# Optimization experiments

Measured on AMD Instinct MI355X. Metric: run time of the kernel, lower is better.

The kernel has to match this reference:

```python
import jax, jax.numpy as jnp
import numpy as np

IN_CH = 128
OUT_CH = 128
MODES = 16
T = 32
N = 32768
SCALE = 1.0 / (IN_CH * OUT_CH)  # TIME_CONV mode


def setup_inputs() -> dict:
    key = jax.random.key(0)
    k_x, k_w = jax.random.split(key)
    x = jax.random.normal(k_x, (T, N, IN_CH), dtype=jnp.float32)
    # nn.Parameter(scale * torch.rand(in, out, modes, 2)) — real/imag stacked in last dim
    weights = SCALE * jax.random.uniform(k_w, (IN_CH, OUT_CH, MODES, 2), dtype=jnp.float32)
    return {"x": x, "weights": weights}


def reference(x, weights):
    # x: [T, N, C_in]; weights: [C_in, C_out, modes, 2]
    w_c = weights[..., 0] + 1j * weights[..., 1]           # [i, o, m] complex
    x_ft = jnp.fft.rfft(x, axis=0)                          # [T//2+1, N, C_in] complex
    out_ft = jnp.einsum('mni,iom->mno', x_ft[:MODES], w_c)  # [modes, N, C_out] complex
    out = jnp.fft.irfft(out_ft, n=T, axis=0)                # [T, N, C_out] real
    return out
```

## Files before the change

kernel.cpp:

```cpp
#include <hip/hip_runtime.h>
#include <math.h>

typedef short bf16x8 __attribute__((ext_vector_type(8)));
typedef float f32x4  __attribute__((ext_vector_type(4)));

#define TT 32
#define MM 16
#define CC 128
#define NPT 32768
#define NC 4194304
#define BN 16

#define XF_OFF   0
#define OF_OFF   131072
#define OF_STRIDE 80
#define DT_OFF   151552
#define TABC_OFF 153600
#define TABS_OFF 155648
#define LDS_BYTES 157696

static __device__ __forceinline__ unsigned short f2bf(float f) {
    union { float f; unsigned u; } v; v.f = f;
    unsigned r = v.u + 0x7FFFu + ((v.u >> 16) & 1u);
    return (unsigned short)(r >> 16);
}

__global__ void repack_w(const float* __restrict__ w, bf16x8* __restrict__ wb) {
    int r = blockIdx.x * blockDim.x + threadIdx.x;
    int lane = r & 63;
    int r2 = r >> 6;
    int ot = r2 & 7;
    int r3 = r2 >> 3;
    int ck = r3 & 7;
    int r4 = r3 >> 3;
    int ri = r4 & 1;
    int m  = r4 >> 1;
    int o = ot * 16 + (lane & 15);
    int kbase = ck * 32 + (lane >> 4) * 8;
    bf16x8 v;
    #pragma unroll
    for (int j = 0; j < 8; ++j) {
        int k = kbase + j;
        int i = k >> 1, ko = k & 1;
        const float* wp = w + ((size_t)(i * 128 + o) * 16 + m) * 2;
        float val;
        if (ri == 0) val = ko ? -wp[1] : wp[0];
        else         val = ko ?  wp[0] : wp[1];
        v[j] = (short)f2bf(val);
    }
    wb[r] = v;
}

__global__ __launch_bounds__(1024, 2)
void spectral_mfma(const float* __restrict__ x, const bf16x8* __restrict__ wb,
                   float* __restrict__ out) {
    extern __shared__ char lds[];
    float* tabc = (float*)(lds + TABC_OFF);
    float* tabs = (float*)(lds + TABS_OFF);
    const int tid = threadIdx.x;
    const int n0  = blockIdx.x * BN;

    if (tid < 512) {
        int m = tid & 15, t = tid >> 4;
        float ang = 0.19634954084936207f * (float)((m * t) & 31);
        float s, c; sincosf(ang, &s, &c);
        tabc[t * 16 + m] = c;
        tabs[t * 16 + m] = s;
    }
    {
        int t = tid >> 5, k2 = tid & 31, m = k2 >> 1, ri = k2 & 1;
        float alpha = (m == 0) ? 0.03125f : 0.0625f;
        float ang = 0.19634954084936207f * (float)((m * t) & 31);
        float s, c; sincosf(ang, &s, &c);
        float val = (ri == 0) ? alpha * c : -alpha * s;
        if (m == 0 && ri == 1) val = 0.f;
        *(unsigned short*)(lds + DT_OFF + t * 64 + k2 * 2) = f2bf(val);
    }
    __syncthreads();

    {
        const int i2 = (tid & 63) * 2;
        const int nn = tid >> 6;
        const float* xp = x + (size_t)(n0 + nn) * CC + i2;
        float2 x0  = *(const float2*)(xp);
        float2 x16 = *(const float2*)(xp + (size_t)16 * NC);
        float xrA[16], xiA[16], xrB[16], xiB[16];
        #pragma unroll
        for (int m = 0; m < 16; ++m) {
            float sgn = (m & 1) ? -1.f : 1.f;
            xrA[m] = x0.x + sgn * x16.x;
            xrB[m] = x0.y + sgn * x16.y;
            xiA[m] = 0.f; xiB[m] = 0.f;
        }
        #pragma unroll 3
        for (int t = 1; t <= 15; ++t) {
            float2 a = *(const float2*)(xp + (size_t)t * NC);
            float2 b = *(const float2*)(xp + (size_t)(32 - t) * NC);
            float ex = a.x + b.x, ey = a.y + b.y;
            float ox = a.x - b.x, oy = a.y - b.y;
            float4 c0 = *(const float4*)&tabc[t * 16 + 0];
            float4 c1 = *(const float4*)&tabc[t * 16 + 4];
            float4 c2 = *(const float4*)&tabc[t * 16 + 8];
            float4 c3 = *(const float4*)&tabc[t * 16 + 12];
            float4 s0 = *(const float4*)&tabs[t * 16 + 0];
            float4 s1 = *(const float4*)&tabs[t * 16 + 4];
            float4 s2 = *(const float4*)&tabs[t * 16 + 8];
            float4 s3 = *(const float4*)&tabs[t * 16 + 12];
            float cm[16] = {c0.x,c0.y,c0.z,c0.w, c1.x,c1.y,c1.z,c1.w,
                            c2.x,c2.y,c2.z,c2.w, c3.x,c3.y,c3.z,c3.w};
            float sm[16] = {s0.x,s0.y,s0.z,s0.w, s1.x,s1.y,s1.z,s1.w,
                            s2.x,s2.y,s2.z,s2.w, s3.x,s3.y,s3.z,s3.w};
            #pragma unroll
            for (int m = 0; m < 16; ++m) {
                xrA[m] += ex * cm[m]; xrB[m] += ey * cm[m];
                xiA[m] -= ox * sm[m]; xiB[m] -= oy * sm[m];
            }
        }
        char* xfb = lds + XF_OFF;
        #pragma unroll
        for (int m = 0; m < 16; ++m) {
            unsigned byte = (unsigned)(m * 8192 + nn * 512 + i2 * 4);
            byte ^= (unsigned)((nn & 7) << 4);
            uint2 v;
            v.x = (unsigned)f2bf(xrA[m]) | ((unsigned)f2bf(xiA[m]) << 16);
            v.y = (unsigned)f2bf(xrB[m]) | ((unsigned)f2bf(xiB[m]) << 16);
            *(uint2*)(xfb + byte) = v;
        }
    }
    __syncthreads();

    const int lane = tid & 63;
    const int wid  = tid >> 6;
    const int col  = lane & 15;
    const int kq   = lane >> 4;

    bf16x8 afrag[8];
    {
        char* xfb = lds + XF_OFF;
        const unsigned row = (unsigned)(wid * 8192 + col * 512 + kq * 16);
        const unsigned swz = (unsigned)((col & 7) << 4);
        #pragma unroll
        for (int ck = 0; ck < 8; ++ck) {
            unsigned addr = (row + (unsigned)(ck * 64)) ^ swz;
            afrag[ck] = *(const bf16x8*)(xfb + addr);
        }
    }
    bf16x8 dtf0, dtf1;
    {
        char* dtb = lds + DT_OFF;
        dtf0 = *(const bf16x8*)(dtb + col * 64 + kq * 16);
        dtf1 = *(const bf16x8*)(dtb + (col + 16) * 64 + kq * 16);
    }

    char* ofb = lds + OF_OFF;
    float* outp = out + (size_t)(n0 + wid) * CC + col;

    for (int og = 0; og < 8; ++og) {
        f32x4 accR = {0.f, 0.f, 0.f, 0.f};
        f32x4 accI = {0.f, 0.f, 0.f, 0.f};
        #pragma unroll
        for (int ck = 0; ck < 8; ++ck) {
            bf16x8 bR = wb[(((wid * 2 + 0) * 8 + ck) * 8 + og) * 64 + lane];
            bf16x8 bI = wb[(((wid * 2 + 1) * 8 + ck) * 8 + og) * 64 + lane];
            accR = __builtin_amdgcn_mfma_f32_16x16x32_bf16(afrag[ck], bR, accR, 0, 0, 0);
            accI = __builtin_amdgcn_mfma_f32_16x16x32_bf16(afrag[ck], bI, accI, 0, 0, 0);
        }
        #pragma unroll
        for (int j = 0; j < 4; ++j) {
            int no = (kq * 4 + j) * 16 + col;
            unsigned byte = (unsigned)(no * OF_STRIDE + wid * 4);
            unsigned v = (unsigned)f2bf(accR[j]) | ((unsigned)f2bf(accI[j]) << 16);
            *(unsigned*)(ofb + byte) = v;
        }
        __syncthreads();
        {
            int no0 = wid * 16 + col;
            bf16x8 pf = *(const bf16x8*)(ofb + no0 * OF_STRIDE + kq * 16);
            f32x4 z = {0.f, 0.f, 0.f, 0.f};
            f32x4 c0 = __builtin_amdgcn_mfma_f32_16x16x32_bf16(dtf0, pf, z, 0, 0, 0);
            f32x4 c1 = __builtin_amdgcn_mfma_f32_16x16x32_bf16(dtf1, pf, z, 0, 0, 0);
            float* op = outp + og * 16;
            #pragma unroll
            for (int j = 0; j < 4; ++j) {
                int t0 = kq * 4 + j;
                op[(size_t)t0 * NC]        = c0[j];
                op[(size_t)(t0 + 16) * NC] = c1[j];
            }
        }
        __syncthreads();
    }
}

#define FBN 8
#define FXST 36
__global__ __launch_bounds__(512, 2)
void spectral_fused(const float* __restrict__ x,
                    const float* __restrict__ w,
                    float* __restrict__ out) {
    extern __shared__ float flds[];
    float* xf    = flds;
    float* ftabc = flds + FBN * CC * FXST;
    float* ftabs = ftabc + 512;

    const int tid = threadIdx.x;
    const int n0  = blockIdx.x * FBN;

    {
        const int m = tid >> 5;
        const int t = tid & 31;
        const int k = (m * t) & 31;
        const float ang = 0.19634954084936207f * (float)k;
        float s, c; sincosf(ang, &s, &c);
        ftabc[tid] = c; ftabs[tid] = s;
    }
    __syncthreads();
    {
        const int i   = tid & 127;
        const int nnA = tid >> 7;
        const int nnB = nnA + 4;
        float xra[MM], xia[MM], xrb[MM], xib[MM];
        #pragma unroll
        for (int m = 0; m < MM; ++m) { xra[m]=0.f; xia[m]=0.f; xrb[m]=0.f; xib[m]=0.f; }
        const float* xA = x + (size_t)(n0 + nnA) * CC + i;
        const float* xB = x + (size_t)(n0 + nnB) * CC + i;
        for (int t = 0; t < TT; ++t) {
            const float va = xA[(size_t)t * NC];
            const float vb = xB[(size_t)t * NC];
            #pragma unroll
            for (int m = 0; m < MM; ++m) {
                const float c = ftabc[(m << 5) + t];
                const float s = ftabs[(m << 5) + t];
                xra[m] += va * c;  xia[m] -= va * s;
                xrb[m] += vb * c;  xib[m] -= vb * s;
            }
        }
        float* dA = xf + (size_t)(nnA * CC + i) * FXST;
        float* dB = xf + (size_t)(nnB * CC + i) * FXST;
        #pragma unroll
        for (int j = 0; j < 8; ++j) {
            *(float4*)(dA + 4 * j) = make_float4(xra[2*j], xia[2*j], xra[2*j+1], xia[2*j+1]);
            *(float4*)(dB + 4 * j) = make_float4(xrb[2*j], xib[2*j], xrb[2*j+1], xib[2*j+1]);
        }
    }
    __syncthreads();
    const int o   = tid & 127;
    const int nnA = tid >> 7;
    const int nnB = nnA + 4;
    float ar[MM], ai_[MM], br[MM], bi_[MM];
    #pragma unroll
    for (int m = 0; m < MM; ++m) { ar[m]=0.f; ai_[m]=0.f; br[m]=0.f; bi_[m]=0.f; }
    const float* qa0 = xf + (size_t)(nnA * CC) * FXST;
    const float* qb0 = xf + (size_t)(nnB * CC) * FXST;
    float4 wv[8];
    {
        const float4* wp = (const float4*)(w + (size_t)o * 32);
        #pragma unroll
        for (int j = 0; j < 8; ++j) wv[j] = wp[j];
    }
    for (int i = 0; i < CC; ++i) {
        float4 xa4[8], xb4[8];
        const float4* qa = (const float4*)(qa0 + i * FXST);
        const float4* qb = (const float4*)(qb0 + i * FXST);
        #pragma unroll
        for (int j = 0; j < 8; ++j) { xa4[j] = qa[j]; xb4[j] = qb[j]; }
        float4 wn[8];
        if (i + 1 < CC) {
            const float4* wp = (const float4*)(w + (size_t)((i + 1) * CC + o) * 32);
            #pragma unroll
            for (int j = 0; j < 8; ++j) wn[j] = wp[j];
        }
        #pragma unroll
        for (int j = 0; j < 8; ++j) {
            const int m0 = 2 * j, m1 = 2 * j + 1;
            ar[m0]  += xa4[j].x * wv[j].x - xa4[j].y * wv[j].y;
            ai_[m0] += xa4[j].x * wv[j].y + xa4[j].y * wv[j].x;
            br[m0]  += xb4[j].x * wv[j].x - xb4[j].y * wv[j].y;
            bi_[m0] += xb4[j].x * wv[j].y + xb4[j].y * wv[j].x;
            ar[m1]  += xa4[j].z * wv[j].z - xa4[j].w * wv[j].w;
            ai_[m1] += xa4[j].z * wv[j].w + xa4[j].w * wv[j].z;
            br[m1]  += xb4[j].z * wv[j].z - xb4[j].w * wv[j].w;
            bi_[m1] += xb4[j].z * wv[j].w + xb4[j].w * wv[j].z;
        }
        #pragma unroll
        for (int j = 0; j < 8; ++j) wv[j] = wn[j];
    }
    {
        const float inv = 1.0f / 32.0f;
        const size_t obA = (size_t)(n0 + nnA) * CC + o;
        const size_t obB = (size_t)(n0 + nnB) * CC + o;
        for (int t = 0; t < TT; ++t) {
            float accA = 0.f, accB = 0.f;
            #pragma unroll
            for (int m = 1; m < MM; ++m) {
                const float c = ftabc[(m << 5) + t];
                const float s = ftabs[(m << 5) + t];
                accA += ar[m] * c - ai_[m] * s;
                accB += br[m] * c - bi_[m] * s;
            }
            out[(size_t)t * NC + obA] = (ar[0] + 2.f * accA) * inv;
            out[(size_t)t * NC + obB] = (br[0] + 2.f * accB) * inv;
        }
    }
}

extern "C" void kernel_launch(void* const* d_in, const int* in_sizes, int n_in,
                              void* d_out, int out_size, void* d_ws, size_t ws_size,
                              hipStream_t stream) {
    (void)in_sizes; (void)n_in; (void)out_size;
    const float* x = (const float*)d_in[0];
    const float* w = (const float*)d_in[1];
    float* out     = (float*)d_out;

    if (d_ws != nullptr && ws_size >= (size_t)2 * 1024 * 1024) {
        bf16x8* wbuf = (bf16x8*)d_ws;
        hipLaunchKernelGGL(repack_w, dim3(512), dim3(256), 0, stream, w, wbuf);
        hipLaunchKernelGGL(spectral_mfma, dim3(NPT / BN), dim3(1024), LDS_BYTES, stream,
                           x, wbuf, out);
    } else {
        const size_t lds_bytes = (size_t)(FBN * CC * FXST + 1024) * sizeof(float);
        hipLaunchKernelGGL(spectral_fused, dim3(NPT / FBN), dim3(512), lds_bytes, stream,
                           x, w, out);
    }
}
```

Baseline: 464.7 us.

## Halve block tile to 8 points, shrink LDS and registers for higher occupancy

Reduces the per-block point count from 16 to 8, roughly halving LDS use and per-thread DFT register arrays so more blocks can be resident per CU (launch bounds raised to 8). The weight layout is reordered so each wave streams a contiguous og-major slab, A fragments are loaded from LDS per ck instead of being held in registers, and the inverse-DFT matrix is computed in registers with each half of the waves producing 16 time steps. In exchange the grid doubles, weights are reloaded twice as often per point, and half the lanes go idle during the spectral write-out.

```diff
diff --git a/kernel.cpp b/kernel.cpp
--- a/kernel.cpp
+++ b/kernel.cpp
@@ -9,15 +9,14 @@
 #define CC 128
 #define NPT 32768
 #define NC 4194304
-#define BN 16
+#define BN 8
 
 #define XF_OFF   0
-#define OF_OFF   131072
+#define OF_OFF   65536
 #define OF_STRIDE 80
-#define DT_OFF   151552
-#define TABC_OFF 153600
-#define TABS_OFF 155648
-#define LDS_BYTES 157696
+#define TABC_OFF 75776
+#define TABS_OFF 77824
+#define LDS_BYTES 79872
 
 static __device__ __forceinline__ unsigned short f2bf(float f) {
     union { float f; unsigned u; } v; v.f = f;
@@ -29,13 +28,13 @@
     int r = blockIdx.x * blockDim.x + threadIdx.x;
     int lane = r & 63;
     int r2 = r >> 6;
-    int ot = r2 & 7;
+    int ck = r2 & 7;
     int r3 = r2 >> 3;
-    int ck = r3 & 7;
-    int r4 = r3 >> 3;
-    int ri = r4 & 1;
-    int m  = r4 >> 1;
-    int o = ot * 16 + (lane & 15);
+    int ri = r3 & 1;
+    int r4 = r3 >> 1;
+    int og = r4 & 7;
+    int m  = r4 >> 3;
+    int o = og * 16 + (lane & 15);
     int kbase = ck * 32 + (lane >> 4) * 8;
     bf16x8 v;
     #pragma unroll
@@ -51,7 +50,7 @@
     wb[r] = v;
 }
 
-__global__ __launch_bounds__(1024, 2)
+__global__ __launch_bounds__(1024, 8)
 void spectral_mfma(const float* __restrict__ x, const bf16x8* __restrict__ wb,
                    float* __restrict__ out) {
     extern __shared__ char lds[];
@@ -67,124 +66,110 @@
         tabc[t * 16 + m] = c;
         tabs[t * 16 + m] = s;
     }
-    {
-        int t = tid >> 5, k2 = tid & 31, m = k2 >> 1, ri = k2 & 1;
-        float alpha = (m == 0) ? 0.03125f : 0.0625f;
-        float ang = 0.19634954084936207f * (float)((m * t) & 31);
-        float s, c; sincosf(ang, &s, &c);
-        float val = (ri == 0) ? alpha * c : -alpha * s;
-        if (m == 0 && ri == 1) val = 0.f;
-        *(unsigned short*)(lds + DT_OFF + t * 64 + k2 * 2) = f2bf(val);
-    }
     __syncthreads();
 
     {
-        const int i2 = (tid & 63) * 2;
-        const int nn = tid >> 6;
-        const float* xp = x + (size_t)(n0 + nn) * CC + i2;
-        float2 x0  = *(const float2*)(xp);
-        float2 x16 = *(const float2*)(xp + (size_t)16 * NC);
-        float xrA[16], xiA[16], xrB[16], xiB[16];
+        const int i  = tid & 127;
+        const int nn = tid >> 7;
+        const float* xp = x + (size_t)(n0 + nn) * CC + i;
+        float x0  = xp[0];
+        float x16 = xp[(size_t)16 * NC];
+        float xr[16], xi[16];
         #pragma unroll
         for (int m = 0; m < 16; ++m) {
-            float sgn = (m & 1) ? -1.f : 1.f;
-            xrA[m] = x0.x + sgn * x16.x;
-            xrB[m] = x0.y + sgn * x16.y;
-            xiA[m] = 0.f; xiB[m] = 0.f;
-        }
-        #pragma unroll 3
+            xr[m] = x0 + ((m & 1) ? -x16 : x16);
+            xi[m] = 0.f;
+        }
+        #pragma unroll
         for (int t = 1; t <= 15; ++t) {
-            float2 a = *(const float2*)(xp + (size_t)t * NC);
-            float2 b = *(const float2*)(xp + (size_t)(32 - t) * NC);
-            float ex = a.x + b.x, ey = a.y + b.y;
-            float ox = a.x - b.x, oy = a.y - b.y;
-            float4 c0 = *(const float4*)&tabc[t * 16 + 0];
-            float4 c1 = *(const float4*)&tabc[t * 16 + 4];
-            float4 c2 = *(const float4*)&tabc[t * 16 + 8];
-            float4 c3 = *(const float4*)&tabc[t * 16 + 12];
-            float4 s0 = *(const float4*)&tabs[t * 16 + 0];
-            float4 s1 = *(const float4*)&tabs[t * 16 + 4];
-            float4 s2 = *(const float4*)&tabs[t * 16 + 8];
-            float4 s3 = *(const float4*)&tabs[t * 16 + 12];
-            float cm[16] = {c0.x,c0.y,c0.z,c0.w, c1.x,c1.y,c1.z,c1.w,
-                            c2.x,c2.y,c2.z,c2.w, c3.x,c3.y,c3.z,c3.w};
-            float sm[16] = {s0.x,s0.y,s0.z,s0.w, s1.x,s1.y,s1.z,s1.w,
-                            s2.x,s2.y,s2.z,s2.w, s3.x,s3.y,s3.z,s3.w};
-            #pragma unroll
-            for (int m = 0; m < 16; ++m) {
-                xrA[m] += ex * cm[m]; xrB[m] += ey * cm[m];
-                xiA[m] -= ox * sm[m]; xiB[m] -= oy * sm[m];
+            float a = xp[(size_t)t * NC];
+            float b = xp[(size_t)(32 - t) * NC];
+            float e = a + b, od = a - b;
+            #pragma unroll
+            for (int mh = 0; mh < 16; mh += 8) {
+                float4 c0 = *(const float4*)&tabc[t * 16 + mh];
+                float4 c1 = *(const float4*)&tabc[t * 16 + mh + 4];
+                float4 s0 = *(const float4*)&tabs[t * 16 + mh];
+                float4 s1 = *(const float4*)&tabs[t * 16 + mh + 4];
+                xr[mh+0] += e * c0.x;  xi[mh+0] -= od * s0.x;
+                xr[mh+1] += e * c0.y;  xi[mh+1] -= od * s0.y;
+                xr[mh+2] += e * c0.z;  xi[mh+2] -= od * s0.z;
+                xr[mh+3] += e * c0.w;  xi[mh+3] -= od * s0.w;
+                xr[mh+4] += e * c1.x;  xi[mh+4] -= od * s1.x;
+                xr[mh+5] += e * c1.y;  xi[mh+5] -= od * s1.y;
+                xr[mh+6] += e * c1.z;  xi[mh+6] -= od * s1.z;
+                xr[mh+7] += e * c1.w;  xi[mh+7] -= od * s1.w;
             }
         }
         char* xfb = lds + XF_OFF;
         #pragma unroll
         for (int m = 0; m < 16; ++m) {
-            unsigned byte = (unsigned)(m * 8192 + nn * 512 + i2 * 4);
-            byte ^= (unsigned)((nn & 7) << 4);
-            uint2 v;
-            v.x = (unsigned)f2bf(xrA[m]) | ((unsigned)f2bf(xiA[m]) << 16);
-            v.y = (unsigned)f2bf(xrB[m]) | ((unsigned)f2bf(xiB[m]) << 16);
-            *(uint2*)(xfb + byte) = v;
+            unsigned byte = ((unsigned)(m * 4096 + nn * 512 + i * 4))
+                            ^ ((unsigned)(nn & 7) << 4);
+            unsigned v = (unsigned)f2bf(xr[m]) | ((unsigned)f2bf(xi[m]) << 16);
+            *(unsigned*)(xfb + byte) = v;
         }
     }
     __syncthreads();
 
-    const int lane = tid & 63;
-    const int wid  = tid >> 6;
-    const int col  = lane & 15;
-    const int kq   = lane >> 4;
-
-    bf16x8 afrag[8];
-    {
-        char* xfb = lds + XF_OFF;
-        const unsigned row = (unsigned)(wid * 8192 + col * 512 + kq * 16);
-        const unsigned swz = (unsigned)((col & 7) << 4);
-        #pragma unroll
-        for (int ck = 0; ck < 8; ++ck) {
-            unsigned addr = (row + (unsigned)(ck * 64)) ^ swz;
-            afrag[ck] = *(const bf16x8*)(xfb + addr);
-        }
-    }
-    bf16x8 dtf0, dtf1;
-    {
-        char* dtb = lds + DT_OFF;
-        dtf0 = *(const bf16x8*)(dtb + col * 64 + kq * 16);
-        dtf1 = *(const bf16x8*)(dtb + (col + 16) * 64 + kq * 16);
-    }
-
+    const int lane  = tid & 63;
+    const int wid   = tid >> 6;
+    const int col   = lane & 15;
+    const int kq    = lane >> 4;
+    const int thalf = wid >> 3;
+
+    bf16x8 dtf;
+    {
+        const int t = thalf * 16 + col;
+        #pragma unroll
+        for (int jm = 0; jm < 4; ++jm) {
+            int m = kq * 4 + jm;
+            float alpha = (m == 0) ? 0.03125f : 0.0625f;
+            float ang = 0.19634954084936207f * (float)((m * t) & 31);
+            float s, c; sincosf(ang, &s, &c);
+            dtf[jm * 2 + 0] = (short)f2bf(alpha * c);
+            dtf[jm * 2 + 1] = (m == 0) ? (short)0 : (short)f2bf(-alpha * s);
+        }
+    }
+
+    char* xfb = lds + XF_OFF;
     char* ofb = lds + OF_OFF;
-    float* outp = out + (size_t)(n0 + wid) * CC + col;
+    const unsigned arow = (unsigned)(wid * 4096 + (col & 7) * 512 + kq * 16);
+    const unsigned aswz = (unsigned)((col & 7) << 4);
+    const bf16x8* wbase = wb + (size_t)wid * (8 * 2 * 8 * 64);
+    float* outp = out + (size_t)(n0 + (wid & 7)) * CC + col;
 
     for (int og = 0; og < 8; ++og) {
+        const bf16x8* wog = wbase + (size_t)og * (2 * 8 * 64);
         f32x4 accR = {0.f, 0.f, 0.f, 0.f};
         f32x4 accI = {0.f, 0.f, 0.f, 0.f};
         #pragma unroll
         for (int ck = 0; ck < 8; ++ck) {
-            bf16x8 bR = wb[(((wid * 2 + 0) * 8 + ck) * 8 + og) * 64 + lane];
-            bf16x8 bI = wb[(((wid * 2 + 1) * 8 + ck) * 8 + og) * 64 + lane];
-            accR = __builtin_amdgcn_mfma_f32_16x16x32_bf16(afrag[ck], bR, accR, 0, 0, 0);
-            accI = __builtin_amdgcn_mfma_f32_16x16x32_bf16(afrag[ck], bI, accI, 0, 0, 0);
-        }
-        #pragma unroll
-        for (int j = 0; j < 4; ++j) {
-            int no = (kq * 4 + j) * 16 + col;
-            unsigned byte = (unsigned)(no * OF_STRIDE + wid * 4);
-            unsigned v = (unsigned)f2bf(accR[j]) | ((unsigned)f2bf(accI[j]) << 16);
-            *(unsigned*)(ofb + byte) = v;
+            bf16x8 af = *(const bf16x8*)(xfb + ((arow + (unsigned)(ck * 64)) ^ aswz));
+            bf16x8 bR = wog[(0 * 8 + ck) * 64 + lane];
+            bf16x8 bI = wog[(1 * 8 + ck) * 64 + lane];
+            accR = __builtin_amdgcn_mfma_f32_16x16x32_bf16(af, bR, accR, 0, 0, 0);
+            accI = __builtin_amdgcn_mfma_f32_16x16x32_bf16(af, bI, accI, 0, 0, 0);
+        }
+        if (kq < 2) {
+            #pragma unroll
+            for (int j = 0; j < 4; ++j) {
+                int no = (kq * 4 + j) * 16 + col;
+                unsigned v = (unsigned)f2bf(accR[j]) | ((unsigned)f2bf(accI[j]) << 16);
+                *(unsigned*)(ofb + no * OF_STRIDE + wid * 4) = v;
+            }
         }
         __syncthreads();
         {
-            int no0 = wid * 16 + col;
+            int no0 = (wid & 7) * 16 + col;
             bf16x8 pf = *(const bf16x8*)(ofb + no0 * OF_STRIDE + kq * 16);
             f32x4 z = {0.f, 0.f, 0.f, 0.f};
-            f32x4 c0 = __builtin_amdgcn_mfma_f32_16x16x32_bf16(dtf0, pf, z, 0, 0, 0);
-            f32x4 c1 = __builtin_amdgcn_mfma_f32_16x16x32_bf16(dtf1, pf, z, 0, 0, 0);
+            f32x4 cc = __builtin_amdgcn_mfma_f32_16x16x32_bf16(dtf, pf, z, 0, 0, 0);
             float* op = outp + og * 16;
             #pragma unroll
             for (int j = 0; j < 4; ++j) {
-                int t0 = kq * 4 + j;
-                op[(size_t)t0 * NC]        = c0[j];
-                op[(size_t)(t0 + 16) * NC] = c1[j];
+                int t0 = thalf * 16 + kq * 4 + j;
+                op[(size_t)t0 * NC] = cc[j];
             }
         }
         __syncthreads();
```

After: 551.1 us. +18.6%, slower.

## Halve block to 8 points, cut LDS, recompute DFT fragments in registers

Applied to the files above, without the earlier changes.

Shrinks each block to 8 spatial points and 512 threads so LDS use drops to about 76 KB, allowing more blocks per CU. Each wave now handles two modes per output group and loads A fragments from LDS on demand instead of holding all of them in registers. The weight repack order changes to match. The inverse-DFT fragments are computed directly in registers rather than through an LDS table, and output stores for pairs of channel groups are batched together. The costs are more LDS traffic for A fragments, half the waves idle during the spectral writeback, and a tighter synchronisation structure.

```diff
diff --git a/kernel.cpp b/kernel.cpp
--- a/kernel.cpp
+++ b/kernel.cpp
@@ -2,6 +2,7 @@
 #include <math.h>
 
 typedef short bf16x8 __attribute__((ext_vector_type(8)));
+typedef short bf16x4 __attribute__((ext_vector_type(4)));
 typedef float f32x4  __attribute__((ext_vector_type(4)));
 
 #define TT 32
@@ -9,33 +10,34 @@
 #define CC 128
 #define NPT 32768
 #define NC 4194304
-#define BN 16
+#define BN 8
 
 #define XF_OFF   0
-#define OF_OFF   131072
-#define OF_STRIDE 80
-#define DT_OFF   151552
-#define TABC_OFF 153600
-#define TABS_OFF 155648
-#define LDS_BYTES 157696
+#define OF_OFF   65536
+#define TABC_OFF 73728
+#define TABS_OFF 75776
+#define LDS_BYTES 77824
 
 static __device__ __forceinline__ unsigned short f2bf(float f) {
     union { float f; unsigned u; } v; v.f = f;
     unsigned r = v.u + 0x7FFFu + ((v.u >> 16) & 1u);
     return (unsigned short)(r >> 16);
 }
+static __device__ __forceinline__ unsigned pack2(float lo, float hi) {
+    return (unsigned)f2bf(lo) | ((unsigned)f2bf(hi) << 16);
+}
 
 __global__ void repack_w(const float* __restrict__ w, bf16x8* __restrict__ wb) {
     int r = blockIdx.x * blockDim.x + threadIdx.x;
     int lane = r & 63;
     int r2 = r >> 6;
-    int ot = r2 & 7;
+    int ck = r2 & 7;
     int r3 = r2 >> 3;
-    int ck = r3 & 7;
-    int r4 = r3 >> 3;
-    int ri = r4 & 1;
-    int m  = r4 >> 1;
-    int o = ot * 16 + (lane & 15);
+    int ri = r3 & 1;
+    int r4 = r3 >> 1;
+    int og = r4 & 7;
+    int m  = r4 >> 3;
+    int o = og * 16 + (lane & 15);
     int kbase = ck * 32 + (lane >> 4) * 8;
     bf16x8 v;
     #pragma unroll
@@ -51,7 +53,7 @@
     wb[r] = v;
 }
 
-__global__ __launch_bounds__(1024, 2)
+__global__ __launch_bounds__(512, 2)
 void spectral_mfma(const float* __restrict__ x, const bf16x8* __restrict__ wb,
                    float* __restrict__ out) {
     extern __shared__ char lds[];
@@ -60,27 +62,37 @@
     const int tid = threadIdx.x;
     const int n0  = blockIdx.x * BN;
 
-    if (tid < 512) {
+    const int lane = tid & 63;
+    const int wid  = tid >> 6;
+    const int col  = lane & 15;
+    const int kq   = lane >> 4;
+
+    {
         int m = tid & 15, t = tid >> 4;
-        float ang = 0.19634954084936207f * (float)((m * t) & 31);
-        float s, c; sincosf(ang, &s, &c);
+        float s, c;
+        sincosf(0.19634954084936207f * (float)((m * t) & 31), &s, &c);
         tabc[t * 16 + m] = c;
         tabs[t * 16 + m] = s;
     }
-    {
-        int t = tid >> 5, k2 = tid & 31, m = k2 >> 1, ri = k2 & 1;
+
+    bf16x8 dtf0, dtf1;
+    #pragma unroll
+    for (int jm = 0; jm < 4; ++jm) {
+        int m = kq * 4 + jm;
         float alpha = (m == 0) ? 0.03125f : 0.0625f;
-        float ang = 0.19634954084936207f * (float)((m * t) & 31);
-        float s, c; sincosf(ang, &s, &c);
-        float val = (ri == 0) ? alpha * c : -alpha * s;
-        if (m == 0 && ri == 1) val = 0.f;
-        *(unsigned short*)(lds + DT_OFF + t * 64 + k2 * 2) = f2bf(val);
+        float s, c;
+        sincosf(0.19634954084936207f * (float)((m * col) & 31), &s, &c);
+        dtf0[jm * 2 + 0] = (short)f2bf(alpha * c);
+        dtf0[jm * 2 + 1] = (m == 0) ? (short)0 : (short)f2bf(-alpha * s);
+        sincosf(0.19634954084936207f * (float)((m * (col + 16)) & 31), &s, &c);
+        dtf1[jm * 2 + 0] = (short)f2bf(alpha * c);
+        dtf1[jm * 2 + 1] = (m == 0) ? (short)0 : (short)f2bf(-alpha * s);
     }
     __syncthreads();
 
     {
+        const int nn = tid >> 6;
         const int i2 = (tid & 63) * 2;
-        const int nn = tid >> 6;
         const float* xp = x + (size_t)(n0 + nn) * CC + i2;
         float2 x0  = *(const float2*)(xp);
         float2 x16 = *(const float2*)(xp + (size_t)16 * NC);
@@ -112,79 +124,80 @@
                             s2.x,s2.y,s2.z,s2.w, s3.x,s3.y,s3.z,s3.w};
             #pragma unroll
             for (int m = 0; m < 16; ++m) {
-                xrA[m] += ex * cm[m]; xrB[m] += ey * cm[m];
-                xiA[m] -= ox * sm[m]; xiB[m] -= oy * sm[m];
+                xrA[m] += ex * cm[m];  xiA[m] -= ox * sm[m];
+                xrB[m] += ey * cm[m];  xiB[m] -= oy * sm[m];
             }
         }
         char* xfb = lds + XF_OFF;
         #pragma unroll
         for (int m = 0; m < 16; ++m) {
-            unsigned byte = (unsigned)(m * 8192 + nn * 512 + i2 * 4);
-            byte ^= (unsigned)((nn & 7) << 4);
-            uint2 v;
-            v.x = (unsigned)f2bf(xrA[m]) | ((unsigned)f2bf(xiA[m]) << 16);
-            v.y = (unsigned)f2bf(xrB[m]) | ((unsigned)f2bf(xiB[m]) << 16);
-            *(uint2*)(xfb + byte) = v;
+            unsigned byte = ((unsigned)(m * 4096 + nn * 512 + i2 * 4))
+                            ^ ((unsigned)(nn & 7) << 4);
+            uint2 v2;
+            v2.x = pack2(xrA[m], xiA[m]);
+            v2.y = pack2(xrB[m], xiB[m]);
+            *(uint2*)(xfb + byte) = v2;
         }
     }
     __syncthreads();
 
-    const int lane = tid & 63;
-    const int wid  = tid >> 6;
-    const int col  = lane & 15;
-    const int kq   = lane >> 4;
-
-    bf16x8 afrag[8];
-    {
-        char* xfb = lds + XF_OFF;
-        const unsigned row = (unsigned)(wid * 8192 + col * 512 + kq * 16);
-        const unsigned swz = (unsigned)((col & 7) << 4);
-        #pragma unroll
-        for (int ck = 0; ck < 8; ++ck) {
-            unsigned addr = (row + (unsigned)(ck * 64)) ^ swz;
-            afrag[ck] = *(const bf16x8*)(xfb + addr);
-        }
-    }
-    bf16x8 dtf0, dtf1;
-    {
-        char* dtb = lds + DT_OFF;
-        dtf0 = *(const bf16x8*)(dtb + col * 64 + kq * 16);
-        dtf1 = *(const bf16x8*)(dtb + (col + 16) * 64 + kq * 16);
-    }
-
+    char* xfb = lds + XF_OFF;
     char* ofb = lds + OF_OFF;
+    const unsigned swzA = (unsigned)((col & 7) << 4);
+    const unsigned swzO = (unsigned)((col & 7) << 3);
+    const unsigned rowA = (unsigned)((col & 7) * 512 + kq * 16);
     float* outp = out + (size_t)(n0 + wid) * CC + col;
+    f32x4 sv0 = {0.f,0.f,0.f,0.f}, sv1 = {0.f,0.f,0.f,0.f};
 
     for (int og = 0; og < 8; ++og) {
-        f32x4 accR = {0.f, 0.f, 0.f, 0.f};
-        f32x4 accI = {0.f, 0.f, 0.f, 0.f};
-        #pragma unroll
-        for (int ck = 0; ck < 8; ++ck) {
-            bf16x8 bR = wb[(((wid * 2 + 0) * 8 + ck) * 8 + og) * 64 + lane];
-            bf16x8 bI = wb[(((wid * 2 + 1) * 8 + ck) * 8 + og) * 64 + lane];
-            accR = __builtin_amdgcn_mfma_f32_16x16x32_bf16(afrag[ck], bR, accR, 0, 0, 0);
-            accI = __builtin_amdgcn_mfma_f32_16x16x32_bf16(afrag[ck], bI, accI, 0, 0, 0);
-        }
-        #pragma unroll
-        for (int j = 0; j < 4; ++j) {
-            int no = (kq * 4 + j) * 16 + col;
-            unsigned byte = (unsigned)(no * OF_STRIDE + wid * 4);
-            unsigned v = (unsigned)f2bf(accR[j]) | ((unsigned)f2bf(accI[j]) << 16);
-            *(unsigned*)(ofb + byte) = v;
+        #pragma unroll
+        for (int mm = 0; mm < 2; ++mm) {
+            const int m = wid + mm * 8;
+            const unsigned arow = (unsigned)(m * 4096) + rowA;
+            const bf16x8* wog = wb + (size_t)((m * 8 + og) * 2) * (8 * 64);
+            f32x4 accR = {0.f, 0.f, 0.f, 0.f};
+            f32x4 accI = {0.f, 0.f, 0.f, 0.f};
+            #pragma unroll
+            for (int ck = 0; ck < 8; ++ck) {
+                bf16x8 af = *(const bf16x8*)(xfb + ((arow + (unsigned)(ck * 64)) ^ swzA));
+                bf16x8 bR = wog[(0 * 8 + ck) * 64 + lane];
+                bf16x8 bI = wog[(1 * 8 + ck) * 64 + lane];
+                accR = __builtin_amdgcn_mfma_f32_16x16x32_bf16(af, bR, accR, 0, 0, 0);
+                accI = __builtin_amdgcn_mfma_f32_16x16x32_bf16(af, bI, accI, 0, 0, 0);
+            }
+            if (kq < 2) {
+                #pragma unroll
+                for (int j = 0; j < 4; ++j) {
+                    unsigned no = (unsigned)((kq * 4 + j) * 16 + col);
+                    unsigned addr = no * 64u + (((unsigned)(m * 4)) ^ ((no & 7) << 3));
+                    *(unsigned*)(ofb + addr) = pack2(accR[j], accI[j]);
+                }
+            }
         }
         __syncthreads();
         {
-            int no0 = wid * 16 + col;
-            bf16x8 pf = *(const bf16x8*)(ofb + no0 * OF_STRIDE + kq * 16);
+            unsigned rowb = (unsigned)((wid * 16 + col) * 64);
+            bf16x4 lo = *(const bf16x4*)(ofb + rowb + (((unsigned)(kq * 16)) ^ swzO));
+            bf16x4 hi = *(const bf16x4*)(ofb + rowb + (((unsigned)(kq * 16 + 8)) ^ swzO));
+            bf16x8 pf;
+            #pragma unroll
+            for (int k = 0; k < 4; ++k) { pf[k] = lo[k]; pf[4 + k] = hi[k]; }
             f32x4 z = {0.f, 0.f, 0.f, 0.f};
             f32x4 c0 = __builtin_amdgcn_mfma_f32_16x16x32_bf16(dtf0, pf, z, 0, 0, 0);
             f32x4 c1 = __builtin_amdgcn_mfma_f32_16x16x32_bf16(dtf1, pf, z, 0, 0, 0);
-            float* op = outp + og * 16;
-            #pragma unroll
-            for (int j = 0; j < 4; ++j) {
-                int t0 = kq * 4 + j;
-                op[(size_t)t0 * NC]        = c0[j];
-                op[(size_t)(t0 + 16) * NC] = c1[j];
+            if ((og & 1) == 0) {
+                sv0 = c0; sv1 = c1;
+            } else {
+                float* opE = outp + (og - 1) * 16;
+                float* opO = outp + og * 16;
+                #pragma unroll
+                for (int j = 0; j < 4; ++j) {
+                    int t0 = kq * 4 + j;
+                    opE[(size_t)t0 * NC]        = sv0[j];
+                    opO[(size_t)t0 * NC]        = c0[j];
+                    opE[(size_t)(t0 + 16) * NC] = sv1[j];
+                    opO[(size_t)(t0 + 16) * NC] = c1[j];
+                }
             }
         }
         __syncthreads();
@@ -208,8 +221,7 @@
     {
         const int m = tid >> 5;
         const int t = tid & 31;
-        const int k = (m * t) & 31;
-        const float ang = 0.19634954084936207f * (float)k;
+        const float ang = 0.19634954084936207f * (float)((m * t) & 31);
         float s, c; sincosf(ang, &s, &c);
         ftabc[tid] = c; ftabs[tid] = s;
     }
@@ -314,7 +326,7 @@
     if (d_ws != nullptr && ws_size >= (size_t)2 * 1024 * 1024) {
         bf16x8* wbuf = (bf16x8*)d_ws;
         hipLaunchKernelGGL(repack_w, dim3(512), dim3(256), 0, stream, w, wbuf);
-        hipLaunchKernelGGL(spectral_mfma, dim3(NPT / BN), dim3(1024), LDS_BYTES, stream,
+        hipLaunchKernelGGL(spectral_mfma, dim3(NPT / BN), dim3(512), LDS_BYTES, stream,
                            x, wbuf, out);
     } else {
         const size_t lds_bytes = (size_t)(FBN * CC * FXST + 1024) * sizeof(float);
```

Result: slower. 656.8 us (+41.4%).
